# Kernel optimization log

Measured on AMD Instinct MI355X. Metric: run time of the kernel, lower is better.

The kernel has to match this reference:

```python
import jax, jax.numpy as jnp
import numpy as np

N = 50000
E = 800000
C_IN = 32
C_OUT = 32
K = 8  # number of branch MLPs


def setup_inputs() -> dict:
    key = jax.random.key(0)
    ks = jax.random.split(key, 12)
    x = jax.random.normal(ks[0], (N, C_IN), dtype=jnp.float32)
    pos = jax.random.normal(ks[1], (N, 2), dtype=jnp.float32)
    edge_index = jax.random.randint(ks[2], (2, E), 0, N, dtype=jnp.int32)
    edge_attr = jax.random.normal(ks[3], (E, 4), dtype=jnp.float32)
    edge_weight = jax.random.uniform(ks[4], (E,), dtype=jnp.float32)
    s1 = 1.0 / np.sqrt(C_IN + 4)
    s2 = 1.0 / np.sqrt(C_OUT)
    W1 = jax.random.uniform(ks[5], (K, C_IN + 4, C_OUT), jnp.float32, -s1, s1)
    b1 = jax.random.uniform(ks[6], (K, C_OUT), jnp.float32, -s1, s1)
    W2 = jax.random.uniform(ks[7], (K, C_OUT, C_OUT), jnp.float32, -s2, s2)
    b2 = jax.random.uniform(ks[8], (K, C_OUT), jnp.float32, -s2, s2)
    sr = 1.0 / np.sqrt(C_IN)
    Wr = jax.random.uniform(ks[9], (C_IN, C_OUT), jnp.float32, -sr, sr)
    br = jax.random.uniform(ks[10], (C_OUT,), jnp.float32, -sr, sr)
    return {"x": x, "pos": pos, "edge_index": edge_index, "edge_attr": edge_attr,
            "edge_weight": edge_weight, "W1": W1, "b1": b1, "W2": W2, "b2": b2,
            "Wr": Wr, "br": br}


def reference(x, pos, edge_index, edge_attr, edge_weight, W1, b1, W2, b2, Wr, br):
    src = edge_index[0]  # j (source / neighbor)
    tgt = edge_index[1]  # i (target / aggregation index)

    # gather per-edge features
    x_i = x[tgt]                      # [E, C_IN]
    x_j = x[src]                      # [E, C_IN]
    diff = pos[src] - pos[tgt]        # [E, 2]

    # geometric branch index in [0, 8)
    con0 = (diff[:, 0] > 0).astype(jnp.int32)
    con1 = (diff[:, 1] > 0).astype(jnp.int32)
    con2 = (jnp.abs(diff[:, 0]) - jnp.abs(diff[:, 1]) > 0).astype(jnp.int32)
    idx = con0 + con1 * 2 + con2 * 4  # [E]

    m = jnp.concatenate([x_j - x_i, edge_attr], axis=1)  # [E, C_IN+4]
    # all 8 branch MLPs (Linear->ReLU->Linear->ReLU), then select per edge
    h = jax.nn.relu(jnp.einsum('ec,kcf->ekf', m, W1) + b1[None])   # [E, K, C_OUT]
    f_all = jax.nn.relu(jnp.einsum('ekf,kfg->ekg', h, W2) + b2[None])
    f = jnp.take_along_axis(f_all, idx[:, None, None], axis=1)[:, 0, :]  # [E, C_OUT]
    f = edge_weight[:, None] * f

    # scatter-mean over target nodes
    seg_sum = jax.ops.segment_sum(f, tgt, num_segments=N)
    counts = jax.ops.segment_sum(jnp.ones((f.shape[0],), f.dtype), tgt, num_segments=N)
    out = seg_sum / jnp.maximum(counts, 1.0)[:, None]

    # skip connection
    out = out + x @ Wr + br
    return out
```

## Files before the change

### kernel.cpp

```cpp
#include <hip/hip_runtime.h>

#define N_NODES 50000
#define N_EDGES 800000
#define K_BR    8
#define BCAP    131072
#define MLP_SLOTS (K_BR * BCAP)
#define SCAN_BLOCKS 196
#define BSTRIDE 1024
#define EPT 8
#define P1_BLOCKS 391
#define RB 128
#define RBE 6250


typedef _Float16 h2 __attribute__((ext_vector_type(2)));
typedef _Float16 half8 __attribute__((ext_vector_type(8)));
typedef float f32x4 __attribute__((ext_vector_type(4)));

#define MFMA(a, b, c) __builtin_amdgcn_mfma_f32_16x16x32_f16((a), (b), (c), 0, 0, 0)

#define VAL_MASK 0x3FFFFFFFu
#define FLG_A    0x40000000u
#define FLG_P    0x80000000u


__device__ __forceinline__ int branch_idx(float dx, float dy) {
    return (dx > 0.0f ? 1 : 0) + (dy > 0.0f ? 2 : 0) +
           ((fabsf(dx) - fabsf(dy)) > 0.0f ? 4 : 0);
}

__device__ __forceinline__ unsigned pk_f16pair(float a, float b) {
    h2 p; p.x = (_Float16)a; p.y = (_Float16)b;
    return __builtin_bit_cast(unsigned, p);
}

__device__ __forceinline__ unsigned short f16bits(float a) {
    _Float16 h = (_Float16)a;
    return __builtin_bit_cast(unsigned short, h);
}

__global__ void __launch_bounds__(512) rank_kernel(
    const int* __restrict__ ei, const float* __restrict__ x,
    const float* __restrict__ W1, const float* __restrict__ W2,
    unsigned short* __restrict__ rankB, unsigned char* __restrict__ cntM,
    unsigned* __restrict__ xh, uint4* __restrict__ w1f4, uint4* __restrict__ w2f4) {
    __shared__ unsigned hist[N_NODES / 4];
    int t = threadIdx.x, b = blockIdx.x;
    for (int i = t; i < N_NODES / 4; i += 512) hist[i] = 0;

    int tid = b * 512 + t;
    if (tid < 2048) {
        int L = tid & 63, fl = tid >> 6;
        int nt = fl & 1, kt = (fl >> 1) & 1, k = fl >> 2;
        int quad = L >> 4, col = L & 15;
        unsigned dw[4];
#pragma unroll
        for (int i = 0; i < 4; ++i) {
            float v0 = 0.0f, v1 = 0.0f;
            int k0 = kt * 32 + quad * 8 + 2 * i;
            if (k0 < 36)     v0 = W1[k * 1152 + k0 * 32 + nt * 16 + col];
            if (k0 + 1 < 36) v1 = W1[k * 1152 + (k0 + 1) * 32 + nt * 16 + col];
            dw[i] = pk_f16pair(v0, v1);
        }
        w1f4[tid] = make_uint4(dw[0], dw[1], dw[2], dw[3]);
    } else if (tid < 3072) {
        int u2 = tid - 2048;
        int L = u2 & 63, fl = u2 >> 6;
        int nt = fl & 1, k = fl >> 1;
        int quad = L >> 4, col = L & 15;
        unsigned dw[4];
#pragma unroll
        for (int i = 0; i < 4; ++i) {
            int k0 = quad * 8 + 2 * i;
            dw[i] = pk_f16pair(W2[k * 1024 + k0 * 32 + nt * 16 + col],
                               W2[k * 1024 + (k0 + 1) * 32 + nt * 16 + col]);
        }
        w2f4[u2] = make_uint4(dw[0], dw[1], dw[2], dw[3]);
    }

    __syncthreads();
    int eb = b * RBE;
    for (int it = 0; it < (RBE + 511) / 512; ++it) {
        int r = it * 512 + t;
        if (r < RBE) {
            int e = eb + r;
            int d = ei[N_EDGES + e];
            unsigned sh = (unsigned)(d & 3) * 8u;
            unsigned old = atomicAdd(&hist[d >> 2], 1u << sh);
            rankB[e] = (unsigned short)((old >> sh) & 0xFFu);
            float2 xv = ((const float2*)x)[e];
            xh[e] = pk_f16pair(xv.x, xv.y);
        }
    }
    __syncthreads();
    unsigned* cm = (unsigned*)(cntM + (size_t)b * N_NODES);
    for (int i = t; i < N_NODES / 4; i += 512) cm[i] = hist[i];
}

__global__ void cscan_kernel(const unsigned char* __restrict__ cntM,
                             unsigned short* __restrict__ blkBase,
                             int* __restrict__ cnt, unsigned* __restrict__ ps,
                             int* __restrict__ nodeStart) {
    __shared__ int s[256];
    __shared__ int sh_off;
    int t = threadIdx.x, b = blockIdx.x;
    int d = b * 256 + t;
    int acc = 0;
    if (d < N_NODES) {
#pragma unroll 8
        for (int blk = 0; blk < RB; ++blk) {
            size_t i = (size_t)blk * N_NODES + d;
            int v = cntM[i];
            blkBase[i] = (unsigned short)acc;
            acc += v;
        }
        cnt[d] = acc;
    }
    int v = (d < N_NODES) ? acc : 0;
    s[t] = v;
    __syncthreads();
#pragma unroll
    for (int off = 1; off < 256; off <<= 1) {
        int tmp = (t >= off) ? s[t - off] : 0;
        __syncthreads();
        s[t] += tmp;
        __syncthreads();
    }
    int excl = s[t] - v;
    if (t == 255)
        atomicExch(&ps[b], (unsigned)s[255] | (b == 0 ? FLG_P : FLG_A));
    if (t == 0) sh_off = 0;
    if (t < 64 && b > 0) {
        int off = 0;
        int base = b - 1;
        for (;;) {
            int idx = base - t;
            unsigned w = 0;
            if (idx >= 0) {
                do { w = atomicOr(&ps[idx], 0u); } while (!(w & (FLG_A | FLG_P)));
            }
            bool isP = (w & FLG_P) != 0;
            unsigned long long pm = __ballot(isP);
            int firstP = pm ? (__ffsll((unsigned long long)pm) - 1) : 64;
            int contrib = (idx >= 0 && t <= firstP) ? (int)(w & VAL_MASK) : 0;
#pragma unroll
            for (int sh = 32; sh > 0; sh >>= 1) contrib += __shfl_down(contrib, sh, 64);
            contrib = __shfl(contrib, 0, 64);
            off += contrib;
            if (firstP < 64 || base - 64 < 0) break;
            base -= 64;
        }
        if (t == 0) sh_off = off;
    }
    __syncthreads();
    if (d < N_NODES) nodeStart[d] = excl + sh_off;
}

__global__ void pass1_kernel(const int* __restrict__ ei, const float* __restrict__ pos,
                             const float* __restrict__ ea, const float* __restrict__ ew,
                             const unsigned short* __restrict__ rankB,
                             const unsigned short* __restrict__ blkBase,
                             int* __restrict__ bucketCur,
                             uint4* __restrict__ payload) {
    __shared__ int h[K_BR];
    __shared__ int base[K_BR];
    int t = threadIdx.x;
    if (t < K_BR) h[t] = 0;
    __syncthreads();

    int eBase = blockIdx.x * (256 * EPT);
    int sA[EPT], dA[EPT], krA[EPT], slA[EPT];
#pragma unroll
    for (int it = 0; it < EPT; ++it) {
        int e = eBase + it * 256 + t;
        int s = 0, d = 0, k = 0, rank = 0, slot = 0;
        if (e < N_EDGES) {
            s = ei[e]; d = ei[N_EDGES + e];
            float2 ps2 = ((const float2*)pos)[s];
            float2 pd2 = ((const float2*)pos)[d];
            k = branch_idx(ps2.x - pd2.x, ps2.y - pd2.y);
            rank = atomicAdd(&h[k], 1);
            int bb = e / RBE;
            slot = (int)blkBase[(size_t)bb * N_NODES + d] + (int)rankB[e];
        }
        sA[it] = s; dA[it] = d; krA[it] = (k << 16) | rank; slA[it] = slot;
    }
    __syncthreads();
    if (t < K_BR) base[t] = (h[t] > 0) ? atomicAdd(&bucketCur[t * BSTRIDE], h[t]) : 0;
    __syncthreads();
#pragma unroll
    for (int it = 0; it < EPT; ++it) {
        int e = eBase + it * 256 + t;
        if (e < N_EDGES) {
            int k = krA[it] >> 16, rank = krA[it] & 0xFFFF;
            float4 eav = ((const float4*)ea)[e];
            unsigned ewh = (unsigned)f16bits(ew[e]);
            int idx = (k << 17) + base[k] + rank;
            payload[idx] = make_uint4((unsigned)sA[it] | ((unsigned)dA[it] << 16),
                                      (unsigned)slA[it] | (ewh << 16),
                                      pk_f16pair(eav.x, eav.y),
                                      pk_f16pair(eav.z, eav.w));
        }
    }
}

__global__ void __launch_bounds__(128, 4) mlp_kernel(
    const uint4* __restrict__ payload,
    const unsigned* __restrict__ xh,
    const uint4* __restrict__ w1f4, const float* __restrict__ b1,
    const uint4* __restrict__ w2f4, const float* __restrict__ b2,
    const int* __restrict__ nodeStart,
    const int* __restrict__ bucketFill,
    unsigned short* __restrict__ fbuf) {
    __shared__ uint4 lds4[164];
    char* hreg = (char*)lds4 + (threadIdx.x >> 6) * 1312;

    int t = blockIdx.x * 128 + threadIdx.x;
    int u = __builtin_amdgcn_readfirstlane(t);
    int k = u >> 17;
    int fill = bucketFill[k * BSTRIDE];
    if ((u & (BCAP - 1)) >= fill) return;
    int rel = t & (BCAP - 1);
    bool valid = rel < fill;
    int idx = (k << 17) + min(rel, fill - 1);

    int L = threadIdx.x & 63;
    int quad = L >> 4, col = L & 15;

    uint4 pl = payload[idx];
    int s = (int)(pl.x & 0xFFFFu);
    int d = (int)(pl.x >> 16);
    float whf = (float)__builtin_bit_cast(_Float16, (unsigned short)(pl.y >> 16));
    int slot = valid ? (nodeStart[d] + (int)(pl.y & 0xFFFFu)) : 0;
    int vld = valid ? 1 : 0;

    half8 B1[2][2], B2[2];
#pragma unroll
    for (int kt = 0; kt < 2; ++kt)
#pragma unroll
        for (int nt = 0; nt < 2; ++nt)
            B1[kt][nt] = __builtin_bit_cast(half8, w1f4[((k * 2 + kt) * 2 + nt) * 64 + L]);
#pragma unroll
    for (int nt = 0; nt < 2; ++nt)
        B2[nt] = __builtin_bit_cast(half8, w2f4[(k * 2 + nt) * 64 + L]);
    float b1o0 = b1[k * 32 + col],      b1o1 = b1[k * 32 + 16 + col];
    float b2o0 = b2[k * 32 + col],      b2o1 = b2[k * 32 + 16 + col];

#pragma unroll
    for (int mt = 0; mt < 4; ++mt) {
        int erA = mt * 16 + col;
        int sA = __shfl(s, erA, 64);
        int dAi = __shfl(d, erA, 64);
        unsigned zA = (unsigned)__shfl((int)pl.z, erA, 64);
        unsigned wA = (unsigned)__shfl((int)pl.w, erA, 64);
        uint4 xjv = ((const uint4*)xh)[4 * (size_t)sA + quad];
        uint4 xiv = ((const uint4*)xh)[4 * (size_t)dAi + quad];
        half8 a0 = __builtin_bit_cast(half8, xjv) - __builtin_bit_cast(half8, xiv);
        uint4 a1u = make_uint4(quad == 0 ? zA : 0u, quad == 0 ? wA : 0u, 0u, 0u);
        half8 a1 = __builtin_bit_cast(half8, a1u);

        f32x4 c0 = {b1o0, b1o0, b1o0, b1o0};
        f32x4 c1 = {b1o1, b1o1, b1o1, b1o1};
        c0 = MFMA(a0, B1[0][0], c0);
        c0 = MFMA(a1, B1[1][0], c0);
        c1 = MFMA(a0, B1[0][1], c1);
        c1 = MFMA(a1, B1[1][1], c1);
#pragma unroll
        for (int r = 0; r < 4; ++r) {
            int er = quad * 4 + r;
            *(unsigned short*)(hreg + er * 80 + col * 2)        = f16bits(fmaxf(c0[r], 0.0f));
            *(unsigned short*)(hreg + er * 80 + (16 + col) * 2) = f16bits(fmaxf(c1[r], 0.0f));
        }
        half8 ah = __builtin_bit_cast(half8, *(const uint4*)(hreg + col * 80 + quad * 16));
        f32x4 d0 = {b2o0, b2o0, b2o0, b2o0};
        f32x4 d1 = {b2o1, b2o1, b2o1, b2o1};
        d0 = MFMA(ah, B2[0], d0);
        d1 = MFMA(ah, B2[1], d1);
#pragma unroll
        for (int r = 0; r < 4; ++r) {
            int erC = mt * 16 + quad * 4 + r;
            int slC = __shfl(slot, erC, 64);
            float wC = __shfl(whf, erC, 64);
            int vC = __shfl(vld, erC, 64);
            unsigned short v0 = f16bits(fmaxf(d0[r], 0.0f) * wC);
            unsigned short v1 = f16bits(fmaxf(d1[r], 0.0f) * wC);
            if (vC) {
                unsigned short* orow = fbuf + 32 * (size_t)slC;
                orow[col] = v0;
                orow[16 + col] = v1;
            }
        }
    }
}

__global__ void agg_kernel(const unsigned short* __restrict__ fbuf,
                           const int* __restrict__ nodeStart, const int* __restrict__ deg,
                           const float* __restrict__ x, const float* __restrict__ Wr,
                           const float* __restrict__ br, float* __restrict__ out) {
    int t = blockIdx.x * blockDim.x + threadIdx.x;
    if (t >= N_NODES * 8) return;
    int n = t >> 3, g8 = t & 7;
    int st = nodeStart[n], dg = deg[n];
    const uint2* fb = (const uint2*)fbuf;
    float a0 = 0.0f, a1 = 0.0f, a2 = 0.0f, a3 = 0.0f;
    for (int j = 0; j < dg; ++j) {
        uint2 uu = fb[(size_t)(st + j) * 8 + g8];
        h2 p01 = __builtin_bit_cast(h2, uu.x);
        h2 p23 = __builtin_bit_cast(h2, uu.y);
        a0 += (float)p01.x;
        a1 += (float)p01.y;
        a2 += (float)p23.x;
        a3 += (float)p23.y;
    }
    float inv = 1.0f / (float)max(dg, 1);
    int o = g8 * 4;
    a0 = a0 * inv + br[o];
    a1 = a1 * inv + br[o + 1];
    a2 = a2 * inv + br[o + 2];
    a3 = a3 * inv + br[o + 3];
    const float* xr = x + 32 * (size_t)n;
#pragma unroll
    for (int c = 0; c < 32; ++c) {
        float xv = xr[c];
        a0 = fmaf(xv, Wr[c * 32 + o], a0);
        a1 = fmaf(xv, Wr[c * 32 + o + 1], a1);
        a2 = fmaf(xv, Wr[c * 32 + o + 2], a2);
        a3 = fmaf(xv, Wr[c * 32 + o + 3], a3);
    }
    float4* o4 = (float4*)(out + 32 * (size_t)n + o);
    *o4 = make_float4(a0, a1, a2, a3);
}

extern "C" void kernel_launch(void* const* d_in, const int* in_sizes, int n_in,
                              void* d_out, int out_size, void* d_ws, size_t ws_size,
                              hipStream_t stream) {
    const float* x   = (const float*)d_in[0];
    const float* pos = (const float*)d_in[1];
    const int*   ei  = (const int*)d_in[2];
    const float* ea  = (const float*)d_in[3];
    const float* ew  = (const float*)d_in[4];
    const float* W1  = (const float*)d_in[5];
    const float* b1  = (const float*)d_in[6];
    const float* W2  = (const float*)d_in[7];
    const float* b2  = (const float*)d_in[8];
    const float* Wr  = (const float*)d_in[9];
    const float* br  = (const float*)d_in[10];
    float* out = (float*)d_out;

    char* ws = (char*)d_ws;
    unsigned short* fbuf = (unsigned short*)(ws + 0);
    uint4* payload  = (uint4*)(ws + 51200000);
    int* cnt        = (int*)(ws + 67977216);
    int* bucketCur  = (int*)(ws + 68177216);
    unsigned* psLb  = (unsigned*)(ws + 68209984);
    int* nodeStart  = (int*)(ws + 68210816);
    uint4* w1f4     = (uint4*)(ws + 68410816);
    uint4* w2f4     = (uint4*)(ws + 68443584);
    unsigned* xh    = (unsigned*)(ws + 68459968);
    unsigned short* rankB = (unsigned short*)(ws + 71659968);
    unsigned char* cntM   = (unsigned char*)(ws + 73259968);
    unsigned short* blkBase = (unsigned short*)(ws + 86059968);

    hipMemsetAsync(bucketCur, 0, 33568, stream);

    rank_kernel<<<RB, 512, 0, stream>>>(ei, x, W1, W2, rankB, cntM, xh, w1f4, w2f4);
    cscan_kernel<<<SCAN_BLOCKS, 256, 0, stream>>>(cntM, blkBase, cnt, psLb, nodeStart);
    pass1_kernel<<<P1_BLOCKS, 256, 0, stream>>>(ei, pos, ea, ew, rankB, blkBase,
                                                bucketCur, payload);
    mlp_kernel<<<MLP_SLOTS / 128, 128, 0, stream>>>(payload, xh, w1f4, b1, w2f4, b2,
                                                    nodeStart, bucketCur, fbuf);
    agg_kernel<<<(N_NODES * 8 + 255) / 256, 256, 0, stream>>>(fbuf, nodeStart, cnt,
                                                              x, Wr, br, out);
}
```

Baseline: 185.6 us.

## Fold memset into rank kernel, stage count matrix in LDS, widen aggregation to wave-per-node

Removes the separate hipMemsetAsync by zeroing bucket cursors and scan flags inside the first block of rank_kernel. cscan_kernel now loads its 128x256 byte count tile into LDS with coalesced 32-bit reads before the serial per-node scan, instead of doing strided byte loads from global memory. agg_kernel switches from 8 threads per node to a 64-lane wave per node: four edge groups each sum two channels, the skip matmul is split across the four groups, and the partial sums are combined with shuffles. The intent is to cut launch overhead, uncoalesced byte traffic and per-thread serial edge loops, at the cost of more threads and cross-lane reductions in aggregation. The in-kernel zeroing depends on the later kernels running after rank_kernel on the same stream.

```diff
diff --git a/kernel.cpp b/kernel.cpp
--- a/kernel.cpp
+++ b/kernel.cpp
@@ -43,10 +43,16 @@
     const int* __restrict__ ei, const float* __restrict__ x,
     const float* __restrict__ W1, const float* __restrict__ W2,
     unsigned short* __restrict__ rankB, unsigned char* __restrict__ cntM,
-    unsigned* __restrict__ xh, uint4* __restrict__ w1f4, uint4* __restrict__ w2f4) {
+    unsigned* __restrict__ xh, uint4* __restrict__ w1f4, uint4* __restrict__ w2f4,
+    int* __restrict__ bucketCur, unsigned* __restrict__ ps) {
     __shared__ unsigned hist[N_NODES / 4];
     int t = threadIdx.x, b = blockIdx.x;
     for (int i = t; i < N_NODES / 4; i += 512) hist[i] = 0;
+
+    if (b == 0) {
+        if (t < K_BR) bucketCur[t * BSTRIDE] = 0;
+        if (t < SCAN_BLOCKS) ps[t] = 0;
+    }
 
     int tid = b * 512 + t;
     if (tid < 2048) {
@@ -101,17 +107,27 @@
                              unsigned short* __restrict__ blkBase,
                              int* __restrict__ cnt, unsigned* __restrict__ ps,
                              int* __restrict__ nodeStart) {
+    __shared__ unsigned char cmLds[RB * 256];
     __shared__ int s[256];
     __shared__ int sh_off;
     int t = threadIdx.x, b = blockIdx.x;
-    int d = b * 256 + t;
+    int d0 = b * 256;
+    int d = d0 + t;
+#pragma unroll
+    for (int it = 0; it < RB / 4; ++it) {
+        int i = it * 256 + t;
+        int row = i >> 6;
+        int w = i & 63;
+        ((unsigned*)cmLds)[row * 64 + w] =
+            *(const unsigned*)(cntM + (size_t)row * N_NODES + d0 + (w << 2));
+    }
+    __syncthreads();
     int acc = 0;
     if (d < N_NODES) {
 #pragma unroll 8
         for (int blk = 0; blk < RB; ++blk) {
-            size_t i = (size_t)blk * N_NODES + d;
-            int v = cntM[i];
-            blkBase[i] = (unsigned short)acc;
+            int v = cmLds[blk * 256 + t];
+            blkBase[(size_t)blk * N_NODES + d] = (unsigned short)acc;
             acc += v;
         }
         cnt[d] = acc;
@@ -297,38 +313,37 @@
                            const int* __restrict__ nodeStart, const int* __restrict__ deg,
                            const float* __restrict__ x, const float* __restrict__ Wr,
                            const float* __restrict__ br, float* __restrict__ out) {
-    int t = blockIdx.x * blockDim.x + threadIdx.x;
-    if (t >= N_NODES * 8) return;
-    int n = t >> 3, g8 = t & 7;
-    int st = nodeStart[n], dg = deg[n];
-    const uint2* fb = (const uint2*)fbuf;
-    float a0 = 0.0f, a1 = 0.0f, a2 = 0.0f, a3 = 0.0f;
-    for (int j = 0; j < dg; ++j) {
-        uint2 uu = fb[(size_t)(st + j) * 8 + g8];
-        h2 p01 = __builtin_bit_cast(h2, uu.x);
-        h2 p23 = __builtin_bit_cast(h2, uu.y);
-        a0 += (float)p01.x;
-        a1 += (float)p01.y;
-        a2 += (float)p23.x;
-        a3 += (float)p23.y;
+    int gw = (blockIdx.x * blockDim.x + threadIdx.x) >> 6;
+    if (gw >= N_NODES) return;
+    int l = threadIdx.x & 63;
+    int q = l >> 4, cp = l & 15;
+    int st = nodeStart[gw], dg = deg[gw];
+    float a0 = 0.0f, a1 = 0.0f;
+    for (int j = q; j < dg; j += 4) {
+        unsigned uu = *(const unsigned*)(fbuf + (size_t)(st + j) * 32 + 2 * cp);
+        h2 p = __builtin_bit_cast(h2, uu);
+        a0 += (float)p.x;
+        a1 += (float)p.y;
     }
     float inv = 1.0f / (float)max(dg, 1);
-    int o = g8 * 4;
-    a0 = a0 * inv + br[o];
-    a1 = a1 * inv + br[o + 1];
-    a2 = a2 * inv + br[o + 2];
-    a3 = a3 * inv + br[o + 3];
-    const float* xr = x + 32 * (size_t)n;
-#pragma unroll
-    for (int c = 0; c < 32; ++c) {
-        float xv = xr[c];
-        a0 = fmaf(xv, Wr[c * 32 + o], a0);
-        a1 = fmaf(xv, Wr[c * 32 + o + 1], a1);
-        a2 = fmaf(xv, Wr[c * 32 + o + 2], a2);
-        a3 = fmaf(xv, Wr[c * 32 + o + 3], a3);
-    }
-    float4* o4 = (float4*)(out + 32 * (size_t)n + o);
-    *o4 = make_float4(a0, a1, a2, a3);
+    int c0 = 2 * cp;
+    float p0 = a0 * inv + (q == 0 ? br[c0] : 0.0f);
+    float p1 = a1 * inv + (q == 0 ? br[c0 + 1] : 0.0f);
+    const float* xr = x + 32 * (size_t)gw + q * 8;
+#pragma unroll
+    for (int kk = 0; kk < 8; ++kk) {
+        float xv = xr[kk];
+        p0 = fmaf(xv, Wr[(q * 8 + kk) * 32 + c0], p0);
+        p1 = fmaf(xv, Wr[(q * 8 + kk) * 32 + c0 + 1], p1);
+    }
+    p0 += __shfl_xor(p0, 16, 64);
+    p0 += __shfl_xor(p0, 32, 64);
+    p1 += __shfl_xor(p1, 16, 64);
+    p1 += __shfl_xor(p1, 32, 64);
+    if (q == 0) {
+        float2 o = make_float2(p0, p1);
+        *(float2*)(out + 32 * (size_t)gw + c0) = o;
+    }
 }
 
 extern "C" void kernel_launch(void* const* d_in, const int* in_sizes, int n_in,
@@ -361,14 +376,13 @@
     unsigned char* cntM   = (unsigned char*)(ws + 73259968);
     unsigned short* blkBase = (unsigned short*)(ws + 86059968);
 
-    hipMemsetAsync(bucketCur, 0, 33568, stream);
-
-    rank_kernel<<<RB, 512, 0, stream>>>(ei, x, W1, W2, rankB, cntM, xh, w1f4, w2f4);
+    rank_kernel<<<RB, 512, 0, stream>>>(ei, x, W1, W2, rankB, cntM, xh, w1f4, w2f4,
+                                        bucketCur, psLb);
     cscan_kernel<<<SCAN_BLOCKS, 256, 0, stream>>>(cntM, blkBase, cnt, psLb, nodeStart);
     pass1_kernel<<<P1_BLOCKS, 256, 0, stream>>>(ei, pos, ea, ew, rankB, blkBase,
                                                 bucketCur, payload);
     mlp_kernel<<<MLP_SLOTS / 128, 128, 0, stream>>>(payload, xh, w1f4, b1, w2f4, b2,
                                                     nodeStart, bucketCur, fbuf);
-    agg_kernel<<<(N_NODES * 8 + 255) / 256, 256, 0, stream>>>(fbuf, nodeStart, cnt,
-                                                              x, Wr, br, out);
-}
+    agg_kernel<<<(N_NODES * 64) / 256, 256, 0, stream>>>(fbuf, nodeStart, cnt,
+                                                         x, Wr, br, out);
+}
```

Result: no change. 186.2 us (+0.3%).
